# Performance work log

Hardware: AMD Instinct MI355X
Metric: run time of the kernel (lower is better)

The kernel has to match this reference:

```python
import jax, jax.numpy as jnp
import numpy as np

N, E, F_IN, HID, HEADS, OUT, G = 50000, 800000, 128, 64, 4, 10, 64
NEG_SLOPE = 0.2


def _glorot(key, shape):
    fan = shape[0] + shape[-1]
    lim = np.sqrt(6.0 / fan)
    return jax.random.uniform(key, shape, jnp.float32, -lim, lim)


def setup_inputs() -> dict:
    key = jax.random.key(0)
    ks = jax.random.split(key, 20)
    x = jax.random.normal(ks[0], (N, F_IN), jnp.float32)
    edge_index = jax.random.randint(ks[1], (2, E), 0, N, jnp.int64)
    batch = jnp.sort(jax.random.randint(ks[2], (N,), 0, G, jnp.int64))
    inp = {"x": x, "edge_index": edge_index, "batch": batch}
    # layer 1: in=F_IN, heads=HEADS, out=HID
    inp["W1"] = _glorot(ks[3], (F_IN, HEADS * HID))
    inp["b1"] = jnp.zeros((HEADS * HID,), jnp.float32)
    inp["as1"] = _glorot(ks[4], (HEADS, HID))
    inp["ad1"] = _glorot(ks[5], (HEADS, HID))
    # layer 2: in=HEADS*HID, heads=HEADS, out=HID
    inp["W2"] = _glorot(ks[6], (HEADS * HID, HEADS * HID))
    inp["b2"] = jnp.zeros((HEADS * HID,), jnp.float32)
    inp["as2"] = _glorot(ks[7], (HEADS, HID))
    inp["ad2"] = _glorot(ks[8], (HEADS, HID))
    # layer 3: in=HEADS*HID, heads=1, out=HID
    inp["W3"] = _glorot(ks[9], (HEADS * HID, HID))
    inp["b3"] = jnp.zeros((HID,), jnp.float32)
    inp["as3"] = _glorot(ks[10], (1, HID))
    inp["ad3"] = _glorot(ks[11], (1, HID))
    # MLP head [HID, HID, OUT]
    inp["Wm1"] = _glorot(ks[12], (HID, HID))
    inp["bm1"] = jnp.zeros((HID,), jnp.float32)
    inp["Wm2"] = _glorot(ks[13], (HID, OUT))
    inp["bm2"] = jnp.zeros((OUT,), jnp.float32)
    return inp


def _gat_layer(x, src, dst, W, b, att_src, att_dst):
    # x: [N, Fin]; att_*: [H, C]
    H, C = att_src.shape
    h = (x @ W).reshape(N, H, C)
    a_src = jnp.einsum("nhc,hc->nh", h, att_src)
    a_dst = jnp.einsum("nhc,hc->nh", h, att_dst)
    alpha = jax.nn.leaky_relu(a_src[src] + a_dst[dst], NEG_SLOPE)  # [E', H]
    amax = jax.ops.segment_max(alpha, dst, num_segments=N)
    alpha = jnp.exp(alpha - amax[dst])
    denom = jax.ops.segment_sum(alpha, dst, num_segments=N)
    alpha = alpha / (denom[dst] + 1e-16)
    msg = h[src] * alpha[:, :, None]  # [E', H, C]
    out = jax.ops.segment_sum(msg, dst, num_segments=N)  # [N, H, C]
    return out.reshape(N, H * C) + b


def reference(x, edge_index, batch, W1, b1, as1, ad1, W2, b2, as2, ad2, W3, b3, as3, ad3, Wm1, bm1, Wm2, bm2):
    # PyG GATConv adds self-loops by default
    loops = jnp.arange(N, dtype=edge_index.dtype)
    src = jnp.concatenate([edge_index[0], loops])
    dst = jnp.concatenate([edge_index[1], loops])
    h = jax.nn.relu(_gat_layer(x, src, dst, W1, b1, as1, ad1))
    h = jax.nn.relu(_gat_layer(h, src, dst, W2, b2, as2, ad2))
    h = jax.nn.relu(_gat_layer(h, src, dst, W3, b3, as3, ad3))
    pooled = jax.ops.segment_sum(h, batch, num_segments=G)  # [G, HID]
    hidden = jax.nn.relu(pooled @ Wm1 + bm1)
    return hidden @ Wm2 + bm2
```

## Files before the change

### kernel.cpp

```cpp
#include <hip/hip_runtime.h>
#include <hip/hip_bf16.h>

#define F_IN   128
#define HID    64
#define HEADS  4
#define OUTD   10
#define NGRP   64

typedef unsigned short u16;
typedef __attribute__((ext_vector_type(8))) short short8;
typedef __attribute__((ext_vector_type(4))) float f32x4;

__device__ __forceinline__ float atomAddF(float* p, float v) {
    return __hip_atomic_fetch_add(p, v, __ATOMIC_RELAXED, __HIP_MEMORY_SCOPE_AGENT);
}
__device__ __forceinline__ float lrelu(float f) { return f > 0.f ? f : 0.2f * f; }
__device__ __forceinline__ float b2f(u16 u) { return __uint_as_float(((unsigned)u) << 16); }
__device__ __forceinline__ u16 f2b(float f) {
    unsigned u = __float_as_uint(f);
    return (u16)((u + 0x7fffu + ((u >> 16) & 1u)) >> 16);
}
__device__ __forceinline__ unsigned fmono(float f) {
    unsigned u = __float_as_uint(f);
    return (u & 0x80000000u) ? ~u : (u | 0x80000000u);
}
__device__ __forceinline__ float funmono(unsigned u) {
    return __uint_as_float((u & 0x80000000u) ? (u & 0x7FFFFFFFu) : ~u);
}

__global__ __launch_bounds__(256) void conv_kernel(const float* __restrict__ in,
                                                   u16* __restrict__ out, int n4) {
    int i = blockIdx.x * 256 + threadIdx.x;
    if (i >= n4) return;
    float4 v = ((const float4*)in)[i];
    uint2 o;
    o.x = (unsigned)f2b(v.x) | ((unsigned)f2b(v.y) << 16);
    o.y = (unsigned)f2b(v.z) | ((unsigned)f2b(v.w) << 16);
    ((uint2*)out)[i] = o;
}

__global__ __launch_bounds__(256) void wtrans_kernel(const float* __restrict__ W,
                                                     u16* __restrict__ Wt, int K, int NC) {
    int i = blockIdx.x * 256 + threadIdx.x;
    if (i >= K * NC) return;
    int n = i / K, k = i - n * K;
    Wt[i] = f2b(W[(size_t)k * NC + n]);
}

template<int K, int NC>
__global__ __launch_bounds__(256) void gemm_bf16_kernel(const u16* __restrict__ A,
                                                        const u16* __restrict__ Bt,
                                                        u16* __restrict__ Hb, int nrows) {
    constexpr int LDA = 40;
    __shared__ u16 As[64][LDA];
    __shared__ u16 Bs[NC][LDA];
    int tid = threadIdx.x;
    int m0 = blockIdx.x * 64;
    int w = tid >> 6, l = tid & 63, lr = l & 15, lk = l >> 4;
    f32x4 acc[NC / 16] = {};
    for (int k0 = 0; k0 < K; k0 += 32) {
        {
            int row = tid >> 2, ks = (tid & 3) * 8;
            int grow = m0 + row;
            short8 av = {};
            if (grow < nrows) av = *(const short8*)&A[(size_t)grow * K + k0 + ks];
            *(short8*)&As[row][ks] = av;
        }
        #pragma unroll
        for (int i = 0; i < NC / 64; i++) {
            int col = (tid >> 2) + 64 * i;
            int ks = (tid & 3) * 8;
            *(short8*)&Bs[col][ks] = *(const short8*)&Bt[(size_t)col * K + k0 + ks];
        }
        __syncthreads();
        short8 af = *(const short8*)&As[16 * w + lr][lk * 8];
        #pragma unroll
        for (int c = 0; c < NC / 16; c++) {
            short8 bf = *(const short8*)&Bs[c * 16 + lr][lk * 8];
            acc[c] = __builtin_amdgcn_mfma_f32_16x16x32_bf16(af, bf, acc[c], 0, 0, 0);
        }
        __syncthreads();
    }
    #pragma unroll
    for (int c = 0; c < NC / 16; c++) {
        #pragma unroll
        for (int j = 0; j < 4; j++) {
            int grow = m0 + 16 * w + lk * 4 + j;
            if (grow < nrows) Hb[(size_t)grow * NC + c * 16 + lr] = f2b(acc[c][j]);
        }
    }
}

template<int HH>
__global__ __launch_bounds__(256) void att_kernel(const u16* __restrict__ Hm,
                                                  const float* __restrict__ as_,
                                                  const float* __restrict__ ad_,
                                                  float* __restrict__ a_src,
                                                  float* __restrict__ a_dst, int n_nodes) {
    int wave = (blockIdx.x * 256 + threadIdx.x) >> 6;
    int lane = threadIdx.x & 63;
    if (wave >= n_nodes) return;
    const u16* hrow = Hm + (size_t)wave * HH * 64;
    #pragma unroll
    for (int hh = 0; hh < HH; hh++) {
        float v = b2f(hrow[hh * 64 + lane]);
        float s = v * as_[hh * 64 + lane];
        float d = v * ad_[hh * 64 + lane];
        #pragma unroll
        for (int off = 32; off; off >>= 1) {
            s += __shfl_xor(s, off, 64);
            d += __shfl_xor(d, off, 64);
        }
        if (lane == 0) { a_src[wave * HH + hh] = s; a_dst[wave * HH + hh] = d; }
    }
}

template<int HH>
__global__ __launch_bounds__(256) void gmax_kernel(const float* __restrict__ a_src,
                                                   unsigned* __restrict__ gmaxu, int n_nodes) {
    float mx[HH];
    #pragma unroll
    for (int h = 0; h < HH; h++) mx[h] = -3.4e38f;
    for (int i = blockIdx.x * 256 + threadIdx.x; i < n_nodes; i += gridDim.x * 256) {
        #pragma unroll
        for (int h = 0; h < HH; h++) mx[h] = fmaxf(mx[h], a_src[i * HH + h]);
    }
    #pragma unroll
    for (int h = 0; h < HH; h++) {
        #pragma unroll
        for (int off = 32; off; off >>= 1) mx[h] = fmaxf(mx[h], __shfl_xor(mx[h], off, 64));
    }
    if ((threadIdx.x & 63) == 0) {
        #pragma unroll
        for (int h = 0; h < HH; h++) atomicMax(&gmaxu[h], fmono(mx[h]));
    }
}

__global__ void count_kernel(const int* __restrict__ ei, int* __restrict__ deg,
                             int E_, int n_nodes) {
    int e = blockIdx.x * 256 + threadIdx.x;
    int tot = E_ + n_nodes;
    if (e >= tot) return;
    int d = (e < E_) ? ei[E_ + e] : e - E_;
    atomicAdd(&deg[d], 1);
}

__global__ __launch_bounds__(256) void scan_reduce_kernel(const int* __restrict__ deg,
                                                          int* __restrict__ bsum, int n) {
    int i = blockIdx.x * 256 + threadIdx.x;
    int v = (i < n) ? deg[i] : 0;
    #pragma unroll
    for (int o = 32; o; o >>= 1) v += __shfl_xor(v, o, 64);
    __shared__ int ws[4];
    if ((threadIdx.x & 63) == 0) ws[threadIdx.x >> 6] = v;
    __syncthreads();
    if (threadIdx.x == 0) bsum[blockIdx.x] = ws[0] + ws[1] + ws[2] + ws[3];
}

__global__ __launch_bounds__(256) void scan_blocksums_kernel(int* __restrict__ bsum, int nb) {
    __shared__ int s[256];
    int t = threadIdx.x;
    int v = (t < nb) ? bsum[t] : 0;
    s[t] = v;
    __syncthreads();
    #pragma unroll
    for (int d = 1; d < 256; d <<= 1) {
        int x = (t >= d) ? s[t - d] : 0;
        __syncthreads();
        s[t] += x;
        __syncthreads();
    }
    if (t < nb) bsum[t] = s[t] - v;
}

__global__ __launch_bounds__(256) void scan_final_kernel(const int* __restrict__ deg,
                                                         const int* __restrict__ bsum,
                                                         int* __restrict__ off, int n) {
    __shared__ int s[256];
    int t = threadIdx.x;
    int i = blockIdx.x * 256 + t;
    int v = (i < n) ? deg[i] : 0;
    s[t] = v;
    __syncthreads();
    #pragma unroll
    for (int d = 1; d < 256; d <<= 1) {
        int x = (t >= d) ? s[t - d] : 0;
        __syncthreads();
        s[t] += x;
        __syncthreads();
    }
    int ex = s[t] - v + bsum[blockIdx.x];
    if (i < n) off[i] = ex;
    if (i == n - 1) off[n] = ex + v;
}

__global__ void fill_kernel(const int* __restrict__ ei, const int* __restrict__ off,
                            int* __restrict__ cursor, int* __restrict__ csr_src,
                            int E_, int n_nodes) {
    int e = blockIdx.x * 256 + threadIdx.x;
    int tot = E_ + n_nodes;
    if (e >= tot) return;
    int s, d;
    if (e < E_) { s = ei[e]; d = ei[E_ + e]; } else { s = d = e - E_; }
    int pos = atomicAdd(&cursor[d], 1);
    csr_src[off[d] + pos] = s;
}

template<int HH, int CPL, bool OUTF32>
__global__ __launch_bounds__(256) void gat_aggr_kernel(const int* __restrict__ off,
                                                       const int* __restrict__ csr_src,
                                                       const u16* __restrict__ Hb,
                                                       const float* __restrict__ a_src,
                                                       const float* __restrict__ a_dst,
                                                       const unsigned* __restrict__ gmaxu,
                                                       const float* __restrict__ bias,
                                                       u16* __restrict__ outb16,
                                                       float* __restrict__ outf32,
                                                       int n_nodes) {
    constexpr int HC = 64 * CPL;
    constexpr int GRP = 64 / HH;
    int d = blockIdx.x * 4 + (threadIdx.x >> 6);
    if (d >= n_nodes) return;
    int lane = threadIdx.x & 63;
    int hh = lane / GRP;
    int o0 = off[d];
    int deg = off[d + 1] - o0;
    float adm = a_dst[d * HH + hh];
    float m = lrelu(funmono(gmaxu[hh]) + adm);

    float den = 0.f;
    float acc[CPL] = {};
    int j = 0;
    for (; j + 4 <= deg; j += 4) {
        int s0 = csr_src[o0 + j + 0];
        int s1 = csr_src[o0 + j + 1];
        int s2 = csr_src[o0 + j + 2];
        int s3 = csr_src[o0 + j + 3];
        if constexpr (CPL == 4) {
            uint2 h0 = *(const uint2*)&Hb[(size_t)s0 * HC + lane * 4];
            uint2 h1 = *(const uint2*)&Hb[(size_t)s1 * HC + lane * 4];
            uint2 h2 = *(const uint2*)&Hb[(size_t)s2 * HC + lane * 4];
            uint2 h3 = *(const uint2*)&Hb[(size_t)s3 * HC + lane * 4];
            float e0 = __expf(lrelu(a_src[s0 * HH + hh] + adm) - m);
            float e1 = __expf(lrelu(a_src[s1 * HH + hh] + adm) - m);
            float e2 = __expf(lrelu(a_src[s2 * HH + hh] + adm) - m);
            float e3 = __expf(lrelu(a_src[s3 * HH + hh] + adm) - m);
            den += (e0 + e1) + (e2 + e3);
            acc[0] += e0 * __uint_as_float(h0.x << 16) + e1 * __uint_as_float(h1.x << 16)
                    + e2 * __uint_as_float(h2.x << 16) + e3 * __uint_as_float(h3.x << 16);
            acc[1] += e0 * __uint_as_float(h0.x & 0xffff0000u) + e1 * __uint_as_float(h1.x & 0xffff0000u)
                    + e2 * __uint_as_float(h2.x & 0xffff0000u) + e3 * __uint_as_float(h3.x & 0xffff0000u);
            acc[2] += e0 * __uint_as_float(h0.y << 16) + e1 * __uint_as_float(h1.y << 16)
                    + e2 * __uint_as_float(h2.y << 16) + e3 * __uint_as_float(h3.y << 16);
            acc[3] += e0 * __uint_as_float(h0.y & 0xffff0000u) + e1 * __uint_as_float(h1.y & 0xffff0000u)
                    + e2 * __uint_as_float(h2.y & 0xffff0000u) + e3 * __uint_as_float(h3.y & 0xffff0000u);
        } else {
            u16 h0 = Hb[(size_t)s0 * HC + lane];
            u16 h1 = Hb[(size_t)s1 * HC + lane];
            u16 h2 = Hb[(size_t)s2 * HC + lane];
            u16 h3 = Hb[(size_t)s3 * HC + lane];
            float e0 = __expf(lrelu(a_src[s0 * HH + hh] + adm) - m);
            float e1 = __expf(lrelu(a_src[s1 * HH + hh] + adm) - m);
            float e2 = __expf(lrelu(a_src[s2 * HH + hh] + adm) - m);
            float e3 = __expf(lrelu(a_src[s3 * HH + hh] + adm) - m);
            den += (e0 + e1) + (e2 + e3);
            acc[0] += e0 * b2f(h0) + e1 * b2f(h1) + e2 * b2f(h2) + e3 * b2f(h3);
        }
    }
    for (; j < deg; j++) {
        int s = csr_src[o0 + j];
        float al = __expf(lrelu(a_src[s * HH + hh] + adm) - m);
        den += al;
        if constexpr (CPL == 4) {
            uint2 hv = *(const uint2*)&Hb[(size_t)s * HC + lane * 4];
            acc[0] += al * __uint_as_float(hv.x << 16);
            acc[1] += al * __uint_as_float(hv.x & 0xffff0000u);
            acc[2] += al * __uint_as_float(hv.y << 16);
            acc[3] += al * __uint_as_float(hv.y & 0xffff0000u);
        } else {
            acc[0] += al * b2f(Hb[(size_t)s * HC + lane]);
        }
    }
    float inv = 1.f / (den + 1e-16f);
    if constexpr (CPL == 4) {
        float4 bv = *(const float4*)&bias[lane * 4];
        float v0 = fmaxf(acc[0] * inv + bv.x, 0.f);
        float v1 = fmaxf(acc[1] * inv + bv.y, 0.f);
        float v2 = fmaxf(acc[2] * inv + bv.z, 0.f);
        float v3 = fmaxf(acc[3] * inv + bv.w, 0.f);
        uint2 o;
        o.x = (unsigned)f2b(v0) | ((unsigned)f2b(v1) << 16);
        o.y = (unsigned)f2b(v2) | ((unsigned)f2b(v3) << 16);
        *(uint2*)&outb16[(size_t)d * HC + lane * 4] = o;
    } else {
        float v = fmaxf(acc[0] * inv + bias[lane], 0.f);
        if constexpr (OUTF32) outf32[(size_t)d * HC + lane] = v;
        else                  outb16[(size_t)d * HC + lane] = f2b(v);
    }
}

__global__ __launch_bounds__(256) void pool_kernel(const float* __restrict__ H3,
                                                   const int* __restrict__ batch,
                                                   float* __restrict__ pooled, int n_nodes) {
    int wave = (blockIdx.x * 256 + threadIdx.x) >> 6;
    int lane = threadIdx.x & 63;
    int nwaves = gridDim.x * 4;
    int chunk = (n_nodes + nwaves - 1) / nwaves;
    int start = wave * chunk;
    int end = min(n_nodes, start + chunk);
    if (start >= end) return;
    int cur = batch[start];
    float acc = 0.f;
    for (int n = start; n < end; n++) {
        int g = batch[n];
        if (g != cur) { atomAddF(&pooled[cur * 64 + lane], acc); acc = 0.f; cur = g; }
        acc += H3[(size_t)n * 64 + lane];
    }
    atomAddF(&pooled[cur * 64 + lane], acc);
}

__global__ __launch_bounds__(64) void mlp_kernel(const float* __restrict__ pooled,
                                                 const float* __restrict__ Wm1,
                                                 const float* __restrict__ bm1,
                                                 const float* __restrict__ Wm2,
                                                 const float* __restrict__ bm2,
                                                 float* __restrict__ out) {
    __shared__ float sp[64], sh[64];
    int g = blockIdx.x, t = threadIdx.x;
    sp[t] = pooled[g * 64 + t];
    __syncthreads();
    float a = bm1[t];
    for (int k = 0; k < 64; k++) a += sp[k] * Wm1[k * 64 + t];
    sh[t] = a > 0.f ? a : 0.f;
    __syncthreads();
    if (t < 10) {
        float o = bm2[t];
        for (int j = 0; j < 64; j++) o += sh[j] * Wm2[j * 10 + t];
        out[g * 10 + t] = o;
    }
}

extern "C" void kernel_launch(void* const* d_in, const int* in_sizes, int n_in,
                              void* d_out, int out_size, void* d_ws, size_t ws_size,
                              hipStream_t stream) {
    const float* x   = (const float*)d_in[0];
    const int*   ei  = (const int*)d_in[1];
    const int*   bat = (const int*)d_in[2];
    const float* W1  = (const float*)d_in[3];
    const float* b1  = (const float*)d_in[4];
    const float* as1 = (const float*)d_in[5];
    const float* ad1 = (const float*)d_in[6];
    const float* W2  = (const float*)d_in[7];
    const float* b2  = (const float*)d_in[8];
    const float* as2 = (const float*)d_in[9];
    const float* ad2 = (const float*)d_in[10];
    const float* W3  = (const float*)d_in[11];
    const float* b3  = (const float*)d_in[12];
    const float* as3 = (const float*)d_in[13];
    const float* ad3 = (const float*)d_in[14];
    const float* Wm1 = (const float*)d_in[15];
    const float* bm1 = (const float*)d_in[16];
    const float* Wm2 = (const float*)d_in[17];
    const float* bm2 = (const float*)d_in[18];
    float* out = (float*)d_out;

    const int Nn = in_sizes[0] / F_IN;
    const int Ee = in_sizes[1] / 2;
    const int Et = Ee + Nn;

    char* wsp = (char*)d_ws;
    size_t off_b = 0;
    auto alloc = [&](size_t bytes) { void* p = wsp + off_b; off_b += (bytes + 255) & ~(size_t)255; return p; };
    u16*   xb      = (u16*)alloc((size_t)Nn * F_IN * 2);
    u16*   HbA     = (u16*)alloc((size_t)Nn * 256 * 2);
    u16*   HbB     = (u16*)alloc((size_t)Nn * 256 * 2);
    float* Hf      = (float*)alloc((size_t)Nn * HID * 4);
    u16*   Wt1     = (u16*)alloc((size_t)256 * 128 * 2);
    u16*   Wt2     = (u16*)alloc((size_t)256 * 256 * 2);
    u16*   Wt3     = (u16*)alloc((size_t)64 * 256 * 2);
    float* a_src   = (float*)alloc((size_t)Nn * HEADS * 4);
    float* a_dst   = (float*)alloc((size_t)Nn * HEADS * 4);
    unsigned* gmaxu = (unsigned*)alloc(HEADS * 4);
    int*   deg     = (int*)alloc((size_t)Nn * 4);
    int*   bsum    = (int*)alloc((size_t)256 * 4);
    int*   csr_off = (int*)alloc((size_t)(Nn + 1) * 4);
    int*   cursor  = (int*)alloc((size_t)Nn * 4);
    int*   csr_src = (int*)alloc((size_t)Et * 4);
    float* pooled  = (float*)alloc((size_t)NGRP * HID * 4);
    (void)ws_size;

    int n4 = Nn * F_IN / 4;
    conv_kernel<<<(n4 + 255) / 256, 256, 0, stream>>>(x, xb, n4);
    wtrans_kernel<<<(128 * 256 + 255) / 256, 256, 0, stream>>>(W1, Wt1, 128, 256);
    wtrans_kernel<<<(256 * 256 + 255) / 256, 256, 0, stream>>>(W2, Wt2, 256, 256);
    wtrans_kernel<<<(256 * 64 + 255) / 256, 256, 0, stream>>>(W3, Wt3, 256, 64);

    hipMemsetAsync(deg, 0, (size_t)Nn * 4, stream);
    hipMemsetAsync(cursor, 0, (size_t)Nn * 4, stream);
    int eb = (Et + 255) / 256;
    int nb = (Nn + 255) / 256;
    count_kernel<<<eb, 256, 0, stream>>>(ei, deg, Ee, Nn);
    scan_reduce_kernel<<<nb, 256, 0, stream>>>(deg, bsum, Nn);
    scan_blocksums_kernel<<<1, 256, 0, stream>>>(bsum, nb);
    scan_final_kernel<<<nb, 256, 0, stream>>>(deg, bsum, csr_off, Nn);
    fill_kernel<<<eb, 256, 0, stream>>>(ei, csr_off, cursor, csr_src, Ee, Nn);

    const int gemm_blocks = (Nn + 63) / 64;
    const int nodeBlocks = (Nn + 3) / 4;

    auto run_big_layer = [&](const float* b, const float* as_, const float* ad_) {
        att_kernel<4><<<nodeBlocks, 256, 0, stream>>>(HbA, as_, ad_, a_src, a_dst, Nn);
        hipMemsetAsync(gmaxu, 0, HEADS * 4, stream);
        gmax_kernel<4><<<64, 256, 0, stream>>>(a_src, gmaxu, Nn);
        gat_aggr_kernel<4, 4, false><<<nodeBlocks, 256, 0, stream>>>(csr_off, csr_src, HbA,
                                                                     a_src, a_dst, gmaxu, b,
                                                                     HbB, nullptr, Nn);
    };

    gemm_bf16_kernel<128, 256><<<gemm_blocks, 256, 0, stream>>>(xb, Wt1, HbA, Nn);
    run_big_layer(b1, as1, ad1);
    gemm_bf16_kernel<256, 256><<<gemm_blocks, 256, 0, stream>>>(HbB, Wt2, HbA, Nn);
    run_big_layer(b2, as2, ad2);
    gemm_bf16_kernel<256, 64><<<gemm_blocks, 256, 0, stream>>>(HbB, Wt3, HbA, Nn);
    att_kernel<1><<<nodeBlocks, 256, 0, stream>>>(HbA, as3, ad3, a_src, a_dst, Nn);
    hipMemsetAsync(gmaxu, 0, HEADS * 4, stream);
    gmax_kernel<1><<<64, 256, 0, stream>>>(a_src, gmaxu, Nn);
    gat_aggr_kernel<1, 1, true><<<nodeBlocks, 256, 0, stream>>>(csr_off, csr_src, HbA,
                                                                a_src, a_dst, gmaxu, b3,
                                                                nullptr, Hf, Nn);

    hipMemsetAsync(pooled, 0, (size_t)NGRP * HID * 4, stream);
    pool_kernel<<<128, 256, 0, stream>>>(Hf, bat, pooled, Nn);
    mlp_kernel<<<NGRP, 64, 0, stream>>>(pooled, Wm1, bm1, Wm2, bm2, out);
}
```

Before: 468.0 us.

## Retile 256-col GEMM, share edge exps via shuffles, merge memsets

For NC=256, the GEMM now has each wave compute all 64 rows across a 64-column slice, using a 4x4 MFMA register tile. This reuses A and B fragments and cuts LDS fragment reads per MFMA. In the aggregation kernel, each lane computes one of four edge exponentials and broadcasts it with shuffles, so lanes no longer each recompute all four. It also merges the deg/cursor memsets and uses separate gmax slots per layer, dropping three per-layer memsets. The cost is more accumulator registers (64 floats) in the GEMM, which may lower occupancy, plus extra shuffle instructions.

```diff
diff --git a/kernel.cpp b/kernel.cpp
--- a/kernel.cpp
+++ b/kernel.cpp
@@ -57,36 +57,78 @@
     int tid = threadIdx.x;
     int m0 = blockIdx.x * 64;
     int w = tid >> 6, l = tid & 63, lr = l & 15, lk = l >> 4;
-    f32x4 acc[NC / 16] = {};
-    for (int k0 = 0; k0 < K; k0 += 32) {
-        {
-            int row = tid >> 2, ks = (tid & 3) * 8;
-            int grow = m0 + row;
-            short8 av = {};
-            if (grow < nrows) av = *(const short8*)&A[(size_t)grow * K + k0 + ks];
-            *(short8*)&As[row][ks] = av;
-        }
-        #pragma unroll
-        for (int i = 0; i < NC / 64; i++) {
-            int col = (tid >> 2) + 64 * i;
-            int ks = (tid & 3) * 8;
-            *(short8*)&Bs[col][ks] = *(const short8*)&Bt[(size_t)col * K + k0 + ks];
-        }
-        __syncthreads();
-        short8 af = *(const short8*)&As[16 * w + lr][lk * 8];
+    if constexpr (NC == 256) {
+        f32x4 acc[4][4] = {};
+        for (int k0 = 0; k0 < K; k0 += 32) {
+            {
+                int row = tid >> 2, ks = (tid & 3) * 8;
+                int grow = m0 + row;
+                short8 av = {};
+                if (grow < nrows) av = *(const short8*)&A[(size_t)grow * K + k0 + ks];
+                *(short8*)&As[row][ks] = av;
+            }
+            #pragma unroll
+            for (int i = 0; i < 4; i++) {
+                int col = (tid >> 2) + 64 * i;
+                int ks = (tid & 3) * 8;
+                *(short8*)&Bs[col][ks] = *(const short8*)&Bt[(size_t)col * K + k0 + ks];
+            }
+            __syncthreads();
+            short8 a[4], b[4];
+            #pragma unroll
+            for (int mi = 0; mi < 4; mi++) a[mi] = *(const short8*)&As[16 * mi + lr][lk * 8];
+            #pragma unroll
+            for (int ni = 0; ni < 4; ni++) b[ni] = *(const short8*)&Bs[64 * w + 16 * ni + lr][lk * 8];
+            #pragma unroll
+            for (int mi = 0; mi < 4; mi++)
+                #pragma unroll
+                for (int ni = 0; ni < 4; ni++)
+                    acc[mi][ni] = __builtin_amdgcn_mfma_f32_16x16x32_bf16(a[mi], b[ni], acc[mi][ni], 0, 0, 0);
+            __syncthreads();
+        }
+        #pragma unroll
+        for (int mi = 0; mi < 4; mi++) {
+            #pragma unroll
+            for (int j = 0; j < 4; j++) {
+                int grow = m0 + 16 * mi + lk * 4 + j;
+                if (grow < nrows) {
+                    #pragma unroll
+                    for (int ni = 0; ni < 4; ni++)
+                        Hb[(size_t)grow * NC + 64 * w + 16 * ni + lr] = f2b(acc[mi][ni][j]);
+                }
+            }
+        }
+    } else {
+        f32x4 acc[NC / 16] = {};
+        for (int k0 = 0; k0 < K; k0 += 32) {
+            {
+                int row = tid >> 2, ks = (tid & 3) * 8;
+                int grow = m0 + row;
+                short8 av = {};
+                if (grow < nrows) av = *(const short8*)&A[(size_t)grow * K + k0 + ks];
+                *(short8*)&As[row][ks] = av;
+            }
+            {
+                int col = tid >> 2;
+                int ks = (tid & 3) * 8;
+                if (col < NC) *(short8*)&Bs[col][ks] = *(const short8*)&Bt[(size_t)col * K + k0 + ks];
+            }
+            __syncthreads();
+            short8 af = *(const short8*)&As[16 * w + lr][lk * 8];
+            #pragma unroll
+            for (int c = 0; c < NC / 16; c++) {
+                short8 bf = *(const short8*)&Bs[c * 16 + lr][lk * 8];
+                acc[c] = __builtin_amdgcn_mfma_f32_16x16x32_bf16(af, bf, acc[c], 0, 0, 0);
+            }
+            __syncthreads();
+        }
         #pragma unroll
         for (int c = 0; c < NC / 16; c++) {
-            short8 bf = *(const short8*)&Bs[c * 16 + lr][lk * 8];
-            acc[c] = __builtin_amdgcn_mfma_f32_16x16x32_bf16(af, bf, acc[c], 0, 0, 0);
-        }
-        __syncthreads();
-    }
-    #pragma unroll
-    for (int c = 0; c < NC / 16; c++) {
-        #pragma unroll
-        for (int j = 0; j < 4; j++) {
-            int grow = m0 + 16 * w + lk * 4 + j;
-            if (grow < nrows) Hb[(size_t)grow * NC + c * 16 + lr] = f2b(acc[c][j]);
+            #pragma unroll
+            for (int j = 0; j < 4; j++) {
+                int grow = m0 + 16 * w + lk * 4 + j;
+                if (grow < nrows) Hb[(size_t)grow * NC + c * 16 + lr] = f2b(acc[c][j]);
+            }
         }
     }
 }
@@ -223,6 +265,8 @@
     if (d >= n_nodes) return;
     int lane = threadIdx.x & 63;
     int hh = lane / GRP;
+    int g = lane & (GRP - 1);
+    int gb = lane & (64 - GRP);
     int o0 = off[d];
     int deg = off[d + 1] - o0;
     float adm = a_dst[d * HH + hh];
@@ -236,16 +280,19 @@
         int s1 = csr_src[o0 + j + 1];
         int s2 = csr_src[o0 + j + 2];
         int s3 = csr_src[o0 + j + 3];
+        int ssel = s3;
+        if (g == 0) ssel = s0; else if (g == 1) ssel = s1; else if (g == 2) ssel = s2;
+        float e = __expf(lrelu(a_src[ssel * HH + hh] + adm) - m);
+        float e0 = __shfl(e, gb + 0, 64);
+        float e1 = __shfl(e, gb + 1, 64);
+        float e2 = __shfl(e, gb + 2, 64);
+        float e3 = __shfl(e, gb + 3, 64);
+        den += (e0 + e1) + (e2 + e3);
         if constexpr (CPL == 4) {
             uint2 h0 = *(const uint2*)&Hb[(size_t)s0 * HC + lane * 4];
             uint2 h1 = *(const uint2*)&Hb[(size_t)s1 * HC + lane * 4];
             uint2 h2 = *(const uint2*)&Hb[(size_t)s2 * HC + lane * 4];
             uint2 h3 = *(const uint2*)&Hb[(size_t)s3 * HC + lane * 4];
-            float e0 = __expf(lrelu(a_src[s0 * HH + hh] + adm) - m);
-            float e1 = __expf(lrelu(a_src[s1 * HH + hh] + adm) - m);
-            float e2 = __expf(lrelu(a_src[s2 * HH + hh] + adm) - m);
-            float e3 = __expf(lrelu(a_src[s3 * HH + hh] + adm) - m);
-            den += (e0 + e1) + (e2 + e3);
             acc[0] += e0 * __uint_as_float(h0.x << 16) + e1 * __uint_as_float(h1.x << 16)
                     + e2 * __uint_as_float(h2.x << 16) + e3 * __uint_as_float(h3.x << 16);
             acc[1] += e0 * __uint_as_float(h0.x & 0xffff0000u) + e1 * __uint_as_float(h1.x & 0xffff0000u)
@@ -259,11 +306,6 @@
             u16 h1 = Hb[(size_t)s1 * HC + lane];
             u16 h2 = Hb[(size_t)s2 * HC + lane];
             u16 h3 = Hb[(size_t)s3 * HC + lane];
-            float e0 = __expf(lrelu(a_src[s0 * HH + hh] + adm) - m);
-            float e1 = __expf(lrelu(a_src[s1 * HH + hh] + adm) - m);
-            float e2 = __expf(lrelu(a_src[s2 * HH + hh] + adm) - m);
-            float e3 = __expf(lrelu(a_src[s3 * HH + hh] + adm) - m);
-            den += (e0 + e1) + (e2 + e3);
             acc[0] += e0 * b2f(h0) + e1 * b2f(h1) + e2 * b2f(h2) + e3 * b2f(h3);
         }
     }
@@ -380,11 +422,11 @@
     u16*   Wt3     = (u16*)alloc((size_t)64 * 256 * 2);
     float* a_src   = (float*)alloc((size_t)Nn * HEADS * 4);
     float* a_dst   = (float*)alloc((size_t)Nn * HEADS * 4);
-    unsigned* gmaxu = (unsigned*)alloc(HEADS * 4);
-    int*   deg     = (int*)alloc((size_t)Nn * 4);
+    unsigned* gmaxu = (unsigned*)alloc(16 * 4);
+    int*   deg     = (int*)alloc((size_t)Nn * 2 * 4);
+    int*   cursor  = deg + Nn;
     int*   bsum    = (int*)alloc((size_t)256 * 4);
     int*   csr_off = (int*)alloc((size_t)(Nn + 1) * 4);
-    int*   cursor  = (int*)alloc((size_t)Nn * 4);
     int*   csr_src = (int*)alloc((size_t)Et * 4);
     float* pooled  = (float*)alloc((size_t)NGRP * HID * 4);
     (void)ws_size;
@@ -395,8 +437,8 @@
     wtrans_kernel<<<(256 * 256 + 255) / 256, 256, 0, stream>>>(W2, Wt2, 256, 256);
     wtrans_kernel<<<(256 * 64 + 255) / 256, 256, 0, stream>>>(W3, Wt3, 256, 64);
 
-    hipMemsetAsync(deg, 0, (size_t)Nn * 4, stream);
-    hipMemsetAsync(cursor, 0, (size_t)Nn * 4, stream);
+    hipMemsetAsync(deg, 0, (size_t)Nn * 2 * 4, stream);
+    hipMemsetAsync(gmaxu, 0, 16 * 4, stream);
     int eb = (Et + 255) / 256;
     int nb = (Nn + 255) / 256;
     count_kernel<<<eb, 256, 0, stream>>>(ei, deg, Ee, Nn);
@@ -408,25 +450,23 @@
     const int gemm_blocks = (Nn + 63) / 64;
     const int nodeBlocks = (Nn + 3) / 4;
 
-    auto run_big_layer = [&](const float* b, const float* as_, const float* ad_) {
-        att_kernel<4><<<nodeBlocks, 256, 0, stream>>>(HbA, as_, ad_, a_src, a_dst, Nn);
-        hipMemsetAsync(gmaxu, 0, HEADS * 4, stream);
-        gmax_kernel<4><<<64, 256, 0, stream>>>(a_src, gmaxu, Nn);
-        gat_aggr_kernel<4, 4, false><<<nodeBlocks, 256, 0, stream>>>(csr_off, csr_src, HbA,
-                                                                     a_src, a_dst, gmaxu, b,
-                                                                     HbB, nullptr, Nn);
-    };
-
     gemm_bf16_kernel<128, 256><<<gemm_blocks, 256, 0, stream>>>(xb, Wt1, HbA, Nn);
-    run_big_layer(b1, as1, ad1);
+    att_kernel<4><<<nodeBlocks, 256, 0, stream>>>(HbA, as1, ad1, a_src, a_dst, Nn);
+    gmax_kernel<4><<<64, 256, 0, stream>>>(a_src, gmaxu + 0, Nn);
+    gat_aggr_kernel<4, 4, false><<<nodeBlocks, 256, 0, stream>>>(csr_off, csr_src, HbA,
+                                                                 a_src, a_dst, gmaxu + 0, b1,
+                                                                 HbB, nullptr, Nn);
     gemm_bf16_kernel<256, 256><<<gemm_blocks, 256, 0, stream>>>(HbB, Wt2, HbA, Nn);
-    run_big_layer(b2, as2, ad2);
+    att_kernel<4><<<nodeBlocks, 256, 0, stream>>>(HbA, as2, ad2, a_src, a_dst, Nn);
+    gmax_kernel<4><<<64, 256, 0, stream>>>(a_src, gmaxu + 4, Nn);
+    gat_aggr_kernel<4, 4, false><<<nodeBlocks, 256, 0, stream>>>(csr_off, csr_src, HbA,
+                                                                 a_src, a_dst, gmaxu + 4, b2,
+                                                                 HbB, nullptr, Nn);
     gemm_bf16_kernel<256, 64><<<gemm_blocks, 256, 0, stream>>>(HbB, Wt3, HbA, Nn);
     att_kernel<1><<<nodeBlocks, 256, 0, stream>>>(HbA, as3, ad3, a_src, a_dst, Nn);
-    hipMemsetAsync(gmaxu, 0, HEADS * 4, stream);
-    gmax_kernel<1><<<64, 256, 0, stream>>>(a_src, gmaxu, Nn);
+    gmax_kernel<1><<<64, 256, 0, stream>>>(a_src, gmaxu + 8, Nn);
     gat_aggr_kernel<1, 1, true><<<nodeBlocks, 256, 0, stream>>>(csr_off, csr_src, HbA,
-                                                                a_src, a_dst, gmaxu, b3,
+                                                                a_src, a_dst, gmaxu + 8, b3,
                                                                 nullptr, Hf, Nn);
 
     hipMemsetAsync(pooled, 0, (size_t)NGRP * HID * 4, stream);
```

After: 456.7 us. -2.4%, faster.
